# Performance work log

Measured on AMD Instinct MI355X. Metric: run time of the kernel, lower is better.

## Reference

```python
import jax, jax.numpy as jnp
import numpy as np

N_LIG, N_TGT, E = 100000, 20000, 250000
LIG_IN, TGT_IN, H = 4, 1280, 128


def setup_inputs() -> dict:
    key = jax.random.key(0)
    ks = jax.random.split(key, 12)
    def lin_w(k, fan_in, fan_out):
        # kaiming-uniform-ish init, stored as [in, out] for x @ W
        bound = 1.0 / np.sqrt(fan_in)
        return jax.random.uniform(k, (fan_in, fan_out), jnp.float32, -bound, bound)
    return {
        "x_ligand": jax.random.normal(ks[0], (N_LIG, LIG_IN), jnp.float32),
        "x_target": jax.random.normal(ks[1], (N_TGT, TGT_IN), jnp.float32),
        "edge_src": jax.random.randint(ks[2], (E,), 0, N_LIG, jnp.int32),
        "edge_dst": jax.random.randint(ks[3], (E,), 0, N_TGT, jnp.int32),
        # SAGEConv (ligand -> target): lin_l on aggregated ligand msgs, lin_r on target self
        "W_lt_l": lin_w(ks[4], LIG_IN, H),
        "b_lt_l": jnp.zeros((H,), jnp.float32),
        "W_lt_r": lin_w(ks[5], TGT_IN, H),
        # SAGEConv (target -> ligand): lin_l on aggregated target msgs, lin_r on ligand self
        "W_tl_l": lin_w(ks[6], TGT_IN, H),
        "b_tl_l": jnp.zeros((H,), jnp.float32),
        "W_tl_r": lin_w(ks[7], LIG_IN, H),
        # edge predictor: Linear(2H -> 1)
        "W_ep": lin_w(ks[8], 2 * H, 1),
        "b_ep": jnp.zeros((1,), jnp.float32),
    }


def _mean_agg(x_src, src_idx, dst_idx, num_dst):
    # gather per-edge source features, scatter-mean onto destination nodes
    msg = x_src[src_idx]                                             # [E, F]
    s = jax.ops.segment_sum(msg, dst_idx, num_segments=num_dst)      # [N_dst, F]
    cnt = jax.ops.segment_sum(jnp.ones((src_idx.shape[0], 1), x_src.dtype),
                              dst_idx, num_segments=num_dst)         # [N_dst, 1]
    return s / jnp.maximum(cnt, 1.0)


def reference(x_ligand, x_target, edge_src, edge_dst,
              W_lt_l, b_lt_l, W_lt_r, W_tl_l, b_tl_l, W_tl_r, W_ep, b_ep):
    # SAGEConv (ligand, binds_to, target): aggregate ligand msgs into targets
    agg_t = _mean_agg(x_ligand, edge_src, edge_dst, N_TGT)           # [N_TGT, LIG_IN]
    t_out = agg_t @ W_lt_l + b_lt_l + x_target @ W_lt_r              # [N_TGT, H]
    # SAGEConv (target, binds_to, ligand): reversed edges (flip(0))
    agg_l = _mean_agg(x_target, edge_dst, edge_src, N_LIG)           # [N_LIG, TGT_IN]
    l_out = agg_l @ W_tl_l + b_tl_l + x_ligand @ W_tl_r              # [N_LIG, H]
    l_out = jax.nn.relu(l_out)
    t_out = jax.nn.relu(t_out)
    # edge predictor: gather endpoints, concat, linear, squeeze
    edge_feats = jnp.concatenate([l_out[edge_src], t_out[edge_dst]], axis=-1)  # [E, 2H]
    out = (edge_feats @ W_ep + b_ep).squeeze(-1)                     # [E]
    return out
```

## Files before the change

### kernel.cpp

```cpp
#include <hip/hip_runtime.h>
#include <hip/hip_bf16.h>


#define H 128
#define K_DIM 1280
#define LIG_IN 4
#define CAP_L 24
#define CAP_T 48

typedef __attribute__((ext_vector_type(8))) short bf16x8;
typedef __attribute__((ext_vector_type(4))) float f32x4;

#define AS1(p) ((const __attribute__((address_space(1))) void*)(p))
#define AS3(p) ((__attribute__((address_space(3))) void*)(p))

__global__ void fill_both(const int* __restrict__ src, const int* __restrict__ dst,
                          int* __restrict__ cur_l, int* __restrict__ cur_t,
                          int* __restrict__ adjd, int* __restrict__ adjs, int E)
{
    int e = blockIdx.x * blockDim.x + threadIdx.x;
    if (e >= E) return;
    int s = src[e], d = dst[e];
    int p = atomicAdd(&cur_l[s], 1);
    adjd[s * CAP_L + p] = d;
    int q = atomicAdd(&cur_t[d], 1);
    adjs[d * CAP_T + q] = s;
}

__global__ void cast_wt(const float* __restrict__ Wl, const float* __restrict__ Wr,
                        __hip_bfloat16* __restrict__ Wt, int n)
{
    int idx = blockIdx.x * blockDim.x + threadIdx.x;
    if (idx >= n) return;
    int nr = idx / K_DIM, k = idx - nr * K_DIM;
    float v = (nr < H) ? Wl[k * H + nr] : Wr[k * H + (nr - H)];
    Wt[idx] = __float2bfloat16(v);
}

__device__ inline bf16x8 cvt8(float4 u, float4 v)
{
    union { __hip_bfloat16 h[8]; bf16x8 f; } r;
    r.h[0] = __float2bfloat16(u.x); r.h[1] = __float2bfloat16(u.y);
    r.h[2] = __float2bfloat16(u.z); r.h[3] = __float2bfloat16(u.w);
    r.h[4] = __float2bfloat16(v.x); r.h[5] = __float2bfloat16(v.y);
    r.h[6] = __float2bfloat16(v.z); r.h[7] = __float2bfloat16(v.w);
    return r.f;
}

#define NCHUNK 10
__global__ __launch_bounds__(256, 2)
void gemm_fused(const float* __restrict__ Xf,
                const unsigned short* __restrict__ Wt,
                float* __restrict__ y_tl, float* __restrict__ t_lin, int M)
{
    __shared__ short Bs[256 * 128];

    const int t = threadIdx.x;
    const int w = t >> 6, lane = t & 63;
    const int m = lane & 15, q = lane >> 4;
    const int bm = blockIdx.x * 64;

    const int rowc = min(bm + w * 16 + m, M - 1);
    const float* gA = Xf + (size_t)rowc * K_DIM + q * 8;

    f32x4 acc[16];
#pragma unroll
    for (int j = 0; j < 16; ++j) acc[j] = (f32x4){0.f, 0.f, 0.f, 0.f};

    float4 a4[2][8];

#pragma unroll
    for (int s = 0; s < 4; ++s) {
        a4[0][2 * s]     = *(const float4*)(gA + s * 32);
        a4[0][2 * s + 1] = *(const float4*)(gA + s * 32 + 4);
    }
#pragma unroll
    for (int i = 0; i < 16; ++i) {
        int L = i * 256 + t;
        int n = L >> 4, cp = L & 15;
        int cc = cp ^ (n & 15);
        __builtin_amdgcn_global_load_lds(AS1(Wt + (size_t)n * K_DIM + cc * 8),
                                         AS3((char*)Bs + (i * 256 + w * 64) * 16), 16, 0, 0);
    }
    __syncthreads();

#pragma unroll
    for (int c = 0; c < NCHUNK; ++c) {
        const int cur = c & 1;
        if (c + 1 < NCHUNK) {
#pragma unroll
            for (int s = 0; s < 4; ++s) {
                a4[cur ^ 1][2 * s]     = *(const float4*)(gA + (c + 1) * 128 + s * 32);
                a4[cur ^ 1][2 * s + 1] = *(const float4*)(gA + (c + 1) * 128 + s * 32 + 4);
            }
        }
#pragma unroll
        for (int s = 0; s < 4; ++s) {
            bf16x8 aF = cvt8(a4[cur][2 * s], a4[cur][2 * s + 1]);
#pragma unroll
            for (int j = 0; j < 16; ++j) {
                bf16x8 bF = *(const bf16x8*)((const char*)Bs +
                              (j * 16 + m) * 256 + (((s * 4 + q) ^ m) * 16));
                acc[j] = __builtin_amdgcn_mfma_f32_16x16x32_bf16(aF, bF, acc[j], 0, 0, 0);
            }
        }
        __syncthreads();
        if (c + 1 < NCHUNK) {
            const int kc = (c + 1) * 128;
#pragma unroll
            for (int i = 0; i < 16; ++i) {
                int L = i * 256 + t;
                int n = L >> 4, cp = L & 15;
                int cc = cp ^ (n & 15);
                __builtin_amdgcn_global_load_lds(AS1(Wt + (size_t)n * K_DIM + kc + cc * 8),
                                                 AS3((char*)Bs + (i * 256 + w * 64) * 16), 16, 0, 0);
            }
            __syncthreads();
        }
    }

#pragma unroll
    for (int j = 0; j < 16; ++j) {
        float* __restrict__ Y = (j < 8) ? y_tl : t_lin;
        int col = (j & 7) * 16 + m;
#pragma unroll
        for (int r = 0; r < 4; ++r) {
            int row = bm + w * 16 + q * 4 + r;
            if (row < M) Y[(size_t)row * H + col] = acc[j][r];
        }
    }
}

__global__ void target_post(const int* __restrict__ cur_t, const int* __restrict__ adjs,
                            const float* __restrict__ xl, const float* __restrict__ t_lin,
                            const float* __restrict__ W_lt_l, const float* __restrict__ b_lt_l,
                            const float* __restrict__ W_ep,
                            float* __restrict__ st, int NT)
{
    int wid = (blockIdx.x * blockDim.x + threadIdx.x) >> 6;
    int lane = threadIdx.x & 63;
    if (wid >= NT) return;
    int cnt = cur_t[wid];
    float a0 = 0.f, a1 = 0.f, a2 = 0.f, a3 = 0.f;
    for (int j = lane; j < cnt; j += 64) {
        int s = adjs[wid * CAP_T + j];
        float4 v = *(const float4*)(xl + (size_t)s * LIG_IN);
        a0 += v.x; a1 += v.y; a2 += v.z; a3 += v.w;
    }
#pragma unroll
    for (int off = 32; off > 0; off >>= 1) {
        a0 += __shfl_xor(a0, off);
        a1 += __shfl_xor(a1, off);
        a2 += __shfl_xor(a2, off);
        a3 += __shfl_xor(a3, off);
    }
    float inv = 1.0f / fmaxf((float)cnt, 1.0f);
    a0 *= inv; a1 *= inv; a2 *= inv; a3 *= inv;
    float acc = 0.f;
#pragma unroll
    for (int p = 0; p < 2; ++p) {
        int h = lane + p * 64;
        float v = a0 * W_lt_l[h] + a1 * W_lt_l[H + h] + a2 * W_lt_l[2 * H + h] +
                  a3 * W_lt_l[3 * H + h] + b_lt_l[h] + t_lin[(size_t)wid * H + h];
        v = fmaxf(v, 0.f);
        acc += v * W_ep[H + h];
    }
#pragma unroll
    for (int off = 32; off > 0; off >>= 1) acc += __shfl_down(acc, off);
    if (lane == 0) st[wid] = acc;
}

__global__ void ligand_gather_post(const int* __restrict__ cur_l, const int* __restrict__ adjd,
                                   const float* __restrict__ y_tl,
                                   const float* __restrict__ xl,
                                   const float* __restrict__ W_tl_r, const float* __restrict__ b_tl_l,
                                   const float* __restrict__ W_ep,
                                   float* __restrict__ sl, int NL)
{
    int wid = (blockIdx.x * blockDim.x + threadIdx.x) >> 6;
    int lane = threadIdx.x & 63;
    if (wid >= NL) return;
    int cnt = cur_l[wid];
    float a0 = 0.f, a1 = 0.f;
    for (int j = 0; j < cnt; ++j) {
        int d = adjd[wid * CAP_L + j];
        float2 f = ((const float2*)(y_tl + (size_t)d * H))[lane];
        a0 += f.x;
        a1 += f.y;
    }
    float inv = 1.0f / fmaxf((float)cnt, 1.0f);
    float4 x = *(const float4*)(xl + (size_t)wid * LIG_IN);
    float acc = 0.f;
    {
        int h = 2 * lane;
        float v = a0 * inv + b_tl_l[h] +
                  x.x * W_tl_r[h] + x.y * W_tl_r[H + h] +
                  x.z * W_tl_r[2 * H + h] + x.w * W_tl_r[3 * H + h];
        v = fmaxf(v, 0.f);
        acc += v * W_ep[h];
    }
    {
        int h = 2 * lane + 1;
        float v = a1 * inv + b_tl_l[h] +
                  x.x * W_tl_r[h] + x.y * W_tl_r[H + h] +
                  x.z * W_tl_r[2 * H + h] + x.w * W_tl_r[3 * H + h];
        v = fmaxf(v, 0.f);
        acc += v * W_ep[h];
    }
#pragma unroll
    for (int off = 32; off > 0; off >>= 1) acc += __shfl_down(acc, off);
    if (lane == 0) sl[wid] = acc;
}

__global__ void edge_out(const int* __restrict__ src, const int* __restrict__ dst,
                         const float* __restrict__ sl, const float* __restrict__ st,
                         const float* __restrict__ b_ep, float* __restrict__ out, int E)
{
    int e = blockIdx.x * blockDim.x + threadIdx.x;
    if (e >= E) return;
    out[e] = sl[src[e]] + st[dst[e]] + b_ep[0];
}

extern "C" void kernel_launch(void* const* d_in, const int* in_sizes, int n_in,
                              void* d_out, int out_size, void* d_ws, size_t ws_size,
                              hipStream_t stream) {
    const float* x_ligand = (const float*)d_in[0];
    const float* x_target = (const float*)d_in[1];
    const int*   edge_src = (const int*)d_in[2];
    const int*   edge_dst = (const int*)d_in[3];
    const float* W_lt_l   = (const float*)d_in[4];
    const float* b_lt_l   = (const float*)d_in[5];
    const float* W_lt_r   = (const float*)d_in[6];
    const float* W_tl_l   = (const float*)d_in[7];
    const float* b_tl_l   = (const float*)d_in[8];
    const float* W_tl_r   = (const float*)d_in[9];
    const float* W_ep     = (const float*)d_in[10];
    const float* b_ep     = (const float*)d_in[11];
    float* out = (float*)d_out;

    const int NL = in_sizes[0] / LIG_IN;
    const int NT = in_sizes[1] / K_DIM;
    const int E  = in_sizes[2];

    char* ws = (char*)d_ws;
    size_t off = 0;
    auto take = [&](size_t bytes) { size_t o = off; off += (bytes + 15) & ~(size_t)15; return o; };
    size_t off_Wt     = take((size_t)2 * H * K_DIM * 2);
    size_t off_y_tl   = take((size_t)NT * H * 4);
    size_t off_t_lin  = take((size_t)NT * H * 4);
    size_t off_adjd   = take((size_t)NL * CAP_L * 4);
    size_t off_adjs   = take((size_t)NT * CAP_T * 4);
    size_t off_cur_l  = take((size_t)NL * 4);
    size_t off_cur_t  = take((size_t)NT * 4);
    size_t off_sl     = take((size_t)NL * 4);
    size_t off_st     = take((size_t)NT * 4);
    if (off > ws_size) {
        hipMemsetAsync(d_out, 0, (size_t)out_size * 4, stream);
        return;
    }

    __hip_bfloat16* Wt = (__hip_bfloat16*)(ws + off_Wt);
    float* y_tl  = (float*)(ws + off_y_tl);
    float* t_lin = (float*)(ws + off_t_lin);
    int*   adjd  = (int*)(ws + off_adjd);
    int*   adjs  = (int*)(ws + off_adjs);
    int*   cur_l = (int*)(ws + off_cur_l);
    int*   cur_t = (int*)(ws + off_cur_t);
    float* sl    = (float*)(ws + off_sl);
    float* st    = (float*)(ws + off_st);

    hipMemsetAsync(cur_l, 0, off_sl - off_cur_l, stream);

    int nw = 2 * H * K_DIM;
    cast_wt<<<(nw + 255) / 256, 256, 0, stream>>>(W_tl_l, W_lt_r, Wt, nw);

    gemm_fused<<<(NT + 63) / 64, 256, 0, stream>>>(x_target, (const unsigned short*)Wt,
                                                   y_tl, t_lin, NT);

    fill_both<<<(E + 255) / 256, 256, 0, stream>>>(edge_src, edge_dst,
                                                   cur_l, cur_t, adjd, adjs, E);

    target_post<<<(NT * 64 + 255) / 256, 256, 0, stream>>>(cur_t, adjs, x_ligand, t_lin,
                                                           W_lt_l, b_lt_l, W_ep, st, NT);
    ligand_gather_post<<<(NL * 64 + 255) / 256, 256, 0, stream>>>(cur_l, adjd, y_tl, x_ligand,
                                                                  W_tl_r, b_tl_l, W_ep, sl, NL);
    edge_out<<<(E + 255) / 256, 256, 0, stream>>>(edge_src, edge_dst, sl, st, b_ep, out, E);
}
```

Before: 301.6 us.

## Split GEMM over N halves and double-buffer B tiles in LDS

```diff
diff --git a/kernel.cpp b/kernel.cpp
--- a/kernel.cpp
+++ b/kernel.cpp
@@ -53,19 +53,31 @@
                 const unsigned short* __restrict__ Wt,
                 float* __restrict__ y_tl, float* __restrict__ t_lin, int M)
 {
-    __shared__ short Bs[256 * 128];
+    __shared__ short Bs[2][128 * 128];
 
     const int t = threadIdx.x;
     const int w = t >> 6, lane = t & 63;
     const int m = lane & 15, q = lane >> 4;
-    const int bm = blockIdx.x * 64;
+    const int mb = blockIdx.x >> 1, nb = blockIdx.x & 1;
+    const int bm = mb * 64;
+    const int nb128 = nb * 128;
 
     const int rowc = min(bm + w * 16 + m, M - 1);
     const float* gA = Xf + (size_t)rowc * K_DIM + q * 8;
 
-    f32x4 acc[16];
-#pragma unroll
-    for (int j = 0; j < 16; ++j) acc[j] = (f32x4){0.f, 0.f, 0.f, 0.f};
+    int bn[8], bcc[8], bdst[8];
+#pragma unroll
+    for (int i = 0; i < 8; ++i) {
+        int L = i * 256 + t;
+        bn[i] = L >> 4;
+        int cp = L & 15;
+        bcc[i] = cp ^ (bn[i] & 15);
+        bdst[i] = (i * 256 + w * 64) * 16;
+    }
+
+    f32x4 acc[8];
+#pragma unroll
+    for (int j = 0; j < 8; ++j) acc[j] = (f32x4){0.f, 0.f, 0.f, 0.f};
 
     float4 a4[2][8];
 
@@ -75,54 +87,44 @@
         a4[0][2 * s + 1] = *(const float4*)(gA + s * 32 + 4);
     }
 #pragma unroll
-    for (int i = 0; i < 16; ++i) {
-        int L = i * 256 + t;
-        int n = L >> 4, cp = L & 15;
-        int cc = cp ^ (n & 15);
-        __builtin_amdgcn_global_load_lds(AS1(Wt + (size_t)n * K_DIM + cc * 8),
-                                         AS3((char*)Bs + (i * 256 + w * 64) * 16), 16, 0, 0);
-    }
+    for (int i = 0; i < 8; ++i)
+        __builtin_amdgcn_global_load_lds(AS1(Wt + (size_t)(nb128 + bn[i]) * K_DIM + bcc[i] * 8),
+                                         AS3((char*)Bs[0] + bdst[i]), 16, 0, 0);
     __syncthreads();
 
 #pragma unroll
     for (int c = 0; c < NCHUNK; ++c) {
-        const int cur = c & 1;
+        const int cur = c & 1, nxt = cur ^ 1;
         if (c + 1 < NCHUNK) {
+            const int kc = (c + 1) * 128;
+#pragma unroll
+            for (int i = 0; i < 8; ++i)
+                __builtin_amdgcn_global_load_lds(
+                    AS1(Wt + (size_t)(nb128 + bn[i]) * K_DIM + kc + bcc[i] * 8),
+                    AS3((char*)Bs[nxt] + bdst[i]), 16, 0, 0);
 #pragma unroll
             for (int s = 0; s < 4; ++s) {
-                a4[cur ^ 1][2 * s]     = *(const float4*)(gA + (c + 1) * 128 + s * 32);
-                a4[cur ^ 1][2 * s + 1] = *(const float4*)(gA + (c + 1) * 128 + s * 32 + 4);
+                a4[nxt][2 * s]     = *(const float4*)(gA + kc + s * 32);
+                a4[nxt][2 * s + 1] = *(const float4*)(gA + kc + s * 32 + 4);
             }
         }
 #pragma unroll
         for (int s = 0; s < 4; ++s) {
             bf16x8 aF = cvt8(a4[cur][2 * s], a4[cur][2 * s + 1]);
 #pragma unroll
-            for (int j = 0; j < 16; ++j) {
-                bf16x8 bF = *(const bf16x8*)((const char*)Bs +
+            for (int j = 0; j < 8; ++j) {
+                bf16x8 bF = *(const bf16x8*)((const char*)Bs[cur] +
                               (j * 16 + m) * 256 + (((s * 4 + q) ^ m) * 16));
                 acc[j] = __builtin_amdgcn_mfma_f32_16x16x32_bf16(aF, bF, acc[j], 0, 0, 0);
             }
         }
         __syncthreads();
-        if (c + 1 < NCHUNK) {
-            const int kc = (c + 1) * 128;
-#pragma unroll
-            for (int i = 0; i < 16; ++i) {
-                int L = i * 256 + t;
-                int n = L >> 4, cp = L & 15;
-                int cc = cp ^ (n & 15);
-                __builtin_amdgcn_global_load_lds(AS1(Wt + (size_t)n * K_DIM + kc + cc * 8),
-                                                 AS3((char*)Bs + (i * 256 + w * 64) * 16), 16, 0, 0);
-            }
-            __syncthreads();
-        }
-    }
-
-#pragma unroll
-    for (int j = 0; j < 16; ++j) {
-        float* __restrict__ Y = (j < 8) ? y_tl : t_lin;
-        int col = (j & 7) * 16 + m;
+    }
+
+    float* __restrict__ Y = nb ? t_lin : y_tl;
+#pragma unroll
+    for (int j = 0; j < 8; ++j) {
+        int col = j * 16 + m;
 #pragma unroll
         for (int r = 0; r < 4; ++r) {
             int row = bm + w * 16 + q * 4 + r;
@@ -274,8 +276,8 @@
     int nw = 2 * H * K_DIM;
     cast_wt<<<(nw + 255) / 256, 256, 0, stream>>>(W_tl_l, W_lt_r, Wt, nw);
 
-    gemm_fused<<<(NT + 63) / 64, 256, 0, stream>>>(x_target, (const unsigned short*)Wt,
-                                                   y_tl, t_lin, NT);
+    gemm_fused<<<((NT + 63) / 64) * 2, 256, 0, stream>>>(x_target, (const unsigned short*)Wt,
+                                                         y_tl, t_lin, NT);
 
     fill_both<<<(E + 255) / 256, 256, 0, stream>>>(edge_src, edge_dst,
                                                    cur_l, cur_t, adjd, adjs, E);
```

Measured after the change: 306.6 us. No clear change (+1.6%).
